# Kernel tuning notes

Measured on AMD Instinct MI355X. Metric: run time of the kernel, lower is better.

Reference implementation:

```python
import jax, jax.numpy as jnp
import numpy as np

HIDDEN_DIM = 64
EIGS_DIM = 16
N_LAYERS = 2
NUM_USERS = 100000
NUM_ITEMS = 200000
N_NODES = NUM_USERS + NUM_ITEMS
N_EDGES = 1250000
N_PATHS = 14  # 2**(sample_hop+1) - 2 with sample_hop=3
LN_EPS = 1e-5


def setup_inputs() -> dict:
    key = jax.random.key(0)
    k1, k2, k3, k4, k5 = jax.random.split(key, 5)
    return {
        "user_emb": 0.1 * jax.random.normal(k1, (NUM_USERS, HIDDEN_DIM), dtype=jnp.float32),
        "item_emb": 0.1 * jax.random.normal(k2, (NUM_ITEMS, HIDDEN_DIM), dtype=jnp.float32),
        "eigs": jax.random.normal(k3, (N_NODES, EIGS_DIM), dtype=jnp.float32),
        "lambda0": jnp.zeros((N_LAYERS,), dtype=jnp.float32),
        "path_emb_w": jnp.zeros((N_LAYERS, N_PATHS, 1), dtype=jnp.float32),
        "indices": jax.random.randint(k4, (2, N_EDGES), 0, N_NODES, dtype=jnp.int64)
        if jax.config.jax_enable_x64
        else jax.random.randint(k4, (2, N_EDGES), 0, N_NODES, dtype=jnp.int32),
        "path_type": jax.random.randint(k5, (N_EDGES,), 0, N_PATHS, dtype=jnp.int32),
    }


def _layer_norm(x, eps=LN_EPS):
    mu = jnp.mean(x, axis=-1, keepdims=True)
    var = jnp.var(x, axis=-1, keepdims=True)
    return (x - mu) * jax.lax.rsqrt(var + eps)


def _sparse_softmax(row, s, num_nodes):
    # softmax over edges grouped by target-node row index
    m = jax.ops.segment_max(s, row, num_segments=num_nodes)
    e = jnp.exp(s - m[row])
    denom = jax.ops.segment_sum(e, row, num_segments=num_nodes)
    return e / denom[row]


def _attention(y, eigs, row, col, path_type, lam0, pemb):
    sqrt_dim = 1.0 / jnp.sqrt(jnp.float32(HIDDEN_DIM))
    # per-edge q.k score  [E]
    x = jnp.sum(y[row] * y[col], axis=-1) * sqrt_dim
    yeig = jnp.sum(eigs[row] * eigs[col], axis=-1)
    s0 = x + jnp.exp(lam0) * yeig
    s1 = pemb[path_type, 0]
    a0 = _sparse_softmax(row, s0, N_NODES)
    a1 = _sparse_softmax(row, s1, N_NODES)
    a = 0.5 * (a0 + a1)
    # sparse-dense matmul: out[r] = sum_e a_e * v[col_e]
    return jax.ops.segment_sum(a[:, None] * y[col], row, num_segments=N_NODES)


def reference(user_emb, item_emb, eigs, lambda0, path_emb_w, indices, path_type):
    row, col = indices[0], indices[1]
    all_emb = jnp.concatenate([user_emb, item_emb], axis=0)  # [N, d]
    embs = [all_emb]
    for l in range(N_LAYERS):
        y = _layer_norm(all_emb)
        all_emb = _attention(y, eigs, row, col, path_type, lambda0[l], path_emb_w[l])
        embs.append(all_emb)
    light_out = jnp.mean(jnp.stack(embs, axis=1), axis=1)  # [N, d]
    return light_out
```

## Files before the change

### kernel.cpp

```cpp
#include <hip/hip_runtime.h>
#include <hip/hip_bf16.h>

#define HD 64
#define ED 16
#define NU 100000
#define NI 200000
#define NN 300000
#define NE 1250000
#define NP 14

#define RB 512
#define NBKT ((NN + RB - 1) / RB)
#define NR8 (NBKT * RB)
#define A_ITEMS 16
#define A_CHUNK (256 * A_ITEMS)
#define A_BLOCKS ((NE + A_CHUNK - 1) / A_CHUNK)
#define DBINS 64

typedef __hip_bfloat16 bf16;
typedef unsigned short ushort8v __attribute__((ext_vector_type(8)));

__device__ __forceinline__ float bf2f(unsigned short u) {
    union { unsigned int i; float f; } c; c.i = ((unsigned int)u) << 16; return c.f;
}
__device__ __forceinline__ unsigned short f2b(float x) {
    bf16 h = __float2bfloat16(x);
    unsigned short u; __builtin_memcpy(&u, &h, 2); return u;
}

__global__ void ln_kernel(const float* __restrict__ user_emb,
                          const float* __restrict__ item_emb,
                          const float* __restrict__ eigs,
                          bf16* __restrict__ yb,
                          bf16* __restrict__ eb)
{
    const int tid = blockIdx.x * blockDim.x + threadIdx.x;
    const int r   = tid >> 3;
    const int sub = tid & 7;
    if (r >= NN) return;
    const float* src = (r < NU) ? user_emb + (size_t)r * HD
                                : item_emb + (size_t)(r - NU) * HD;
    const float4 lo = *reinterpret_cast<const float4*>(src + sub * 8);
    const float4 hi = *reinterpret_cast<const float4*>(src + sub * 8 + 4);
    float x[8] = {lo.x, lo.y, lo.z, lo.w, hi.x, hi.y, hi.z, hi.w};

    float sm = 0.0f, sq = 0.0f;
#pragma unroll
    for (int j = 0; j < 8; ++j) { sm += x[j]; sq += x[j] * x[j]; }
    sm += __shfl_xor(sm, 1, 64); sq += __shfl_xor(sq, 1, 64);
    sm += __shfl_xor(sm, 2, 64); sq += __shfl_xor(sq, 2, 64);
    sm += __shfl_xor(sm, 4, 64); sq += __shfl_xor(sq, 4, 64);
    const float mu  = sm * (1.0f / 64.0f);
    const float var = sq * (1.0f / 64.0f) - mu * mu;
    const float inv = rsqrtf(var + 1e-5f);

    ushort8v w;
#pragma unroll
    for (int j = 0; j < 8; ++j) w[j] = f2b((x[j] - mu) * inv);
    *reinterpret_cast<ushort8v*>(yb + (size_t)r * HD + sub * 8) = w;

    const float2 ev = *reinterpret_cast<const float2*>(eigs + (size_t)r * ED + sub * 2);
    const unsigned int packed = (unsigned int)f2b(ev.x) | ((unsigned int)f2b(ev.y) << 16);
    *reinterpret_cast<unsigned int*>(eb + (size_t)r * ED + sub * 2) = packed;
}

__global__ void bkt_count_kernel(const int* __restrict__ row,
                                 int* __restrict__ bkt_cnt)
{
    __shared__ int hist[NBKT];
    const int tid = threadIdx.x;
    for (int j = tid; j < NBKT; j += 256) hist[j] = 0;
    __syncthreads();
    const int base = blockIdx.x * A_CHUNK;
#pragma unroll
    for (int i = 0; i < A_ITEMS; ++i) {
        const int idx = base + i * 256 + tid;
        if (idx < NE) atomicAdd(&hist[row[idx] >> 9], 1);
    }
    __syncthreads();
    for (int j = tid; j < NBKT; j += 256) {
        const int h = hist[j];
        if (h) atomicAdd(&bkt_cnt[j], h);
    }
}

__global__ void bkt_scan_kernel(const int* __restrict__ bkt_cnt,
                                int* __restrict__ bkt_base,
                                int* __restrict__ wq_bkt)
{
    __shared__ int s[1024];
    const int t = threadIdx.x;
    const int v = (t < NBKT) ? bkt_cnt[t] : 0;
    s[t] = v;
    __syncthreads();
    for (int off = 1; off < 1024; off <<= 1) {
        int x = (t >= off) ? s[t - off] : 0;
        __syncthreads();
        s[t] += x;
        __syncthreads();
    }
    if (t < NBKT) {
        const int excl = s[t] - v;
        bkt_base[t] = excl;
        wq_bkt[t]   = excl;
        if (t == NBKT - 1) bkt_base[NBKT] = s[t];
    }
}

__global__ void bkt_scatter_kernel(const int* __restrict__ row,
                                   const int* __restrict__ col,
                                   const int* __restrict__ pt,
                                   int* __restrict__ wq_bkt,
                                   int* __restrict__ pairs)
{
    __shared__ int hist[NBKT];
    __shared__ int rbase[NBKT];
    __shared__ int roff[NBKT];
    const int tid = threadIdx.x;
    for (int j = tid; j < NBKT; j += 256) { hist[j] = 0; roff[j] = 0; }
    __syncthreads();

    const int base = blockIdx.x * A_CHUNK;
#pragma unroll
    for (int i = 0; i < A_ITEMS; ++i) {
        const int idx = base + i * 256 + tid;
        if (idx < NE) atomicAdd(&hist[row[idx] >> 9], 1);
    }
    __syncthreads();
    for (int j = tid; j < NBKT; j += 256) {
        const int h = hist[j];
        if (h) rbase[j] = atomicAdd(&wq_bkt[j], h);
    }
    __syncthreads();
#pragma unroll
    for (int i = 0; i < A_ITEMS; ++i) {
        const int idx = base + i * 256 + tid;
        if (idx < NE) {
            const int r = row[idx];
            const int b = r >> 9;
            const int v = col[idx] | (pt[idx] << 19) | ((r & (RB - 1)) << 23);
            const int o = atomicAdd(&roff[b], 1);
            pairs[rbase[b] + o] = v;
        }
    }
}

__global__ void bkt_sort_kernel(const int* __restrict__ bkt_base,
                                const int* __restrict__ pairs,
                                const float* __restrict__ eigs,
                                const bf16* __restrict__ eb,
                                int2* __restrict__ rinfo,
                                int2* __restrict__ epacked)
{
    __shared__ int rcnt[RB], lrp[RB], wq2[RB], ssum[256];
    __shared__ int dhist[DBINS], dbase[DBINS];
    __shared__ int perml[RB];
    __shared__ float estage[RB * ED];
    const int tid = threadIdx.x;
    const int b   = blockIdx.x;
    const int r0  = b * RB;
    const int s   = bkt_base[b];
    const int e   = bkt_base[b + 1];

    for (int j = tid; j < RB; j += 256) { rcnt[j] = 0; wq2[j] = 0; perml[j] = -1; }
    for (int j = tid; j < DBINS; j += 256) dhist[j] = 0;
    for (int k = tid; k < RB * ED; k += 256) {
        const int g = r0 * ED + k;
        estage[k] = (g < NN * ED) ? eigs[g] : 0.0f;
    }
    __syncthreads();

    for (int i = s + tid; i < e; i += 256)
        atomicAdd(&rcnt[(pairs[i] >> 23) & (RB - 1)], 1);
    __syncthreads();

    const int a0 = rcnt[2 * tid], a1 = rcnt[2 * tid + 1];
    ssum[tid] = a0 + a1;
    __syncthreads();
    for (int off = 1; off < 256; off <<= 1) {
        int x = (tid >= off) ? ssum[tid - off] : 0;
        __syncthreads();
        ssum[tid] += x;
        __syncthreads();
    }
    const int excl = ssum[tid] - (a0 + a1);
    lrp[2 * tid]     = excl;
    lrp[2 * tid + 1] = excl + a0;
    __syncthreads();

    const int ra   = r0 + 2 * tid;
    const int bin0 = (a0 < DBINS - 1) ? a0 : (DBINS - 1);
    const int bin1 = (a1 < DBINS - 1) ? a1 : (DBINS - 1);
    if (ra < NN)     atomicAdd(&dhist[bin0], 1);
    if (ra + 1 < NN) atomicAdd(&dhist[bin1], 1);
    __syncthreads();
    ssum[tid] = (tid < DBINS) ? dhist[tid] : 0;
    __syncthreads();
    for (int off = 1; off < DBINS; off <<= 1) {
        int x = (tid >= off) ? ssum[tid - off] : 0;
        __syncthreads();
        ssum[tid] += x;
        __syncthreads();
    }
    if (tid < DBINS) { dbase[tid] = ssum[tid] - dhist[tid]; dhist[tid] = 0; }
    __syncthreads();
    if (ra < NN)     perml[dbase[bin0] + atomicAdd(&dhist[bin0], 1)] = 2 * tid;
    if (ra + 1 < NN) perml[dbase[bin1] + atomicAdd(&dhist[bin1], 1)] = 2 * tid + 1;
    __syncthreads();

    for (int j = tid; j < RB; j += 256) {
        const int rl = perml[j];
        int2 out;
        if (rl >= 0) {
            int dg = rcnt[rl]; if (dg > 0xFFF) dg = 0xFFF;
            out = make_int2(s + lrp[rl], (r0 + rl) | (dg << 19));
        } else {
            out = make_int2(0, -1);
        }
        rinfo[r0 + j] = out;
    }

    for (int i = s + tid; i < e; i += 256) {
        const int v  = pairs[i];
        const int rl = (v >> 23) & (RB - 1);
        const int c  = v & 0x7FFFF;
        const ushort8v* ep = reinterpret_cast<const ushort8v*>(eb + (size_t)c * ED);
        const ushort8v q0 = ep[0], q1 = ep[1];
        const float* er = estage + rl * ED;
        float d = 0.0f;
#pragma unroll
        for (int j = 0; j < 8; ++j) d += bf2f(q0[j]) * er[j];
#pragma unroll
        for (int j = 0; j < 8; ++j) d += bf2f(q1[j]) * er[j + 8];
        const int o   = atomicAdd(&wq2[rl], 1);
        const int pos = s + lrp[rl] + o;
        epacked[pos] = make_int2(v & 0x7FFFFF, __float_as_int(d));
    }
}

template <int LAYER>
__global__ __launch_bounds__(256, 4)
void attn_row_kernel(const bf16* __restrict__ yb,
                     const int2* __restrict__ rinfo,
                     const int2* __restrict__ epacked,
                     const float* __restrict__ lambda0,
                     const float* __restrict__ pemb,
                     const float* __restrict__ user_emb,
                     const float* __restrict__ item_emb,
                     bf16* __restrict__ yb_next,
                     float* __restrict__ io)
{
    __shared__ float e1tab[NP];
    if (threadIdx.x < NP)
        e1tab[threadIdx.x] = __expf(pemb[LAYER * NP + threadIdx.x]);
    __syncthreads();

    const int tid  = blockIdx.x * blockDim.x + threadIdx.x;
    const int g    = tid >> 3;
    const int sub  = tid & 7;
    const int lane = (int)(threadIdx.x & 63);
    const int2 ri  = rinfo[g];
    if (ri.y < 0) return;
    const int r    = ri.y & 0x7FFFF;
    const int deg  = (ri.y >> 19) & 0xFFF;
    if (LAYER == 1 && deg == 0) return;

    const int start = ri.x;
    const float lam = __expf(lambda0[LAYER]);

    float yrf[8];
    {
        ushort8v u = *reinterpret_cast<const ushort8v*>(yb + (size_t)r * HD + sub * 8);
#pragma unroll
        for (int j = 0; j < 8; ++j) yrf[j] = bf2f(u[j]);
    }

    float U0[8], U1[8];
#pragma unroll
    for (int j = 0; j < 8; ++j) { U0[j] = 0.0f; U1[j] = 0.0f; }
    float d0 = 0.0f, d1 = 0.0f;

    const bf16* ybs = yb + (size_t)sub * 8;

    int2 myv = (sub < deg) ? epacked[start + sub] : make_int2(0, 0);
    for (int k0 = 0; k0 < deg; k0 += 8) {
        const bool more = (k0 + 8) < deg;
        int2 nxt = make_int2(0, 0);
        if (more && (k0 + 8 + sub) < deg) nxt = epacked[start + k0 + 8 + sub];

        int   vv[8];
        float ee[8];
#pragma unroll
        for (int kk = 0; kk < 8; ++kk) {
            const int src = (lane & ~7) + kk;
            vv[kk] = __shfl(myv.x, src, 64);
            ee[kk] = __int_as_float(__shfl(myv.y, src, 64));
        }

        const int nb = ((deg - k0) < 8) ? (deg - k0) : 8;

        const bf16* p0 = ybs + (size_t)(vv[0] & 0x7FFFF) * HD;
        const bf16* p1 = ybs + (size_t)(vv[1] & 0x7FFFF) * HD;
        const bf16* p2 = ybs + (size_t)(vv[2] & 0x7FFFF) * HD;
        const bf16* p3 = ybs + (size_t)(vv[3] & 0x7FFFF) * HD;
        const bf16* p4 = ybs + (size_t)(vv[4] & 0x7FFFF) * HD;
        const bf16* p5 = ybs + (size_t)(vv[5] & 0x7FFFF) * HD;
        const bf16* p6 = ybs + (size_t)(vv[6] & 0x7FFFF) * HD;
        const bf16* p7 = ybs + (size_t)(vv[7] & 0x7FFFF) * HD;
        ushort8v u0, u1, u2, u3, u4, u5, u6, u7;
        asm volatile("global_load_dwordx4 %0, %1, off" : "=v"(u0) : "v"(p0));
        asm volatile("global_load_dwordx4 %0, %1, off" : "=v"(u1) : "v"(p1));
        asm volatile("global_load_dwordx4 %0, %1, off" : "=v"(u2) : "v"(p2));
        asm volatile("global_load_dwordx4 %0, %1, off" : "=v"(u3) : "v"(p3));
        asm volatile("global_load_dwordx4 %0, %1, off" : "=v"(u4) : "v"(p4));
        asm volatile("global_load_dwordx4 %0, %1, off" : "=v"(u5) : "v"(p5));
        asm volatile("global_load_dwordx4 %0, %1, off" : "=v"(u6) : "v"(p6));
        asm volatile("global_load_dwordx4 %0, %1, off" : "=v"(u7) : "v"(p7));
        asm volatile("s_waitcnt vmcnt(0)"
                     : "+v"(u0), "+v"(u1), "+v"(u2), "+v"(u3),
                       "+v"(u4), "+v"(u5), "+v"(u6), "+v"(u7));

        auto consume = [&](const ushort8v& uc, int vk, float ek) {
            float yc[8];
            float sdot = 0.0f;
#pragma unroll
            for (int j = 0; j < 8; ++j) { yc[j] = bf2f(uc[j]); sdot += yrf[j] * yc[j]; }
            sdot += __shfl_xor(sdot, 1, 64);
            sdot += __shfl_xor(sdot, 2, 64);
            sdot += __shfl_xor(sdot, 4, 64);
            const float e0 = __expf(sdot * 0.125f + lam * ek);
            const float e1 = e1tab[(vk >> 19) & 15];
            d0 += e0; d1 += e1;
#pragma unroll
            for (int j = 0; j < 8; ++j) {
                U0[j] += e0 * yc[j];
                U1[j] += e1 * yc[j];
            }
        };
        if (nb > 0) consume(u0, vv[0], ee[0]);
        if (nb > 1) consume(u1, vv[1], ee[1]);
        if (nb > 2) consume(u2, vv[2], ee[2]);
        if (nb > 3) consume(u3, vv[3], ee[3]);
        if (nb > 4) consume(u4, vv[4], ee[4]);
        if (nb > 5) consume(u5, vv[5], ee[5]);
        if (nb > 6) consume(u6, vv[6], ee[6]);
        if (nb > 7) consume(u7, vv[7], ee[7]);

        myv = nxt;
    }

    const float i0 = deg ? 0.5f / d0 : 0.0f;
    const float i1 = deg ? 0.5f / d1 : 0.0f;
    float acc[8];
#pragma unroll
    for (int j = 0; j < 8; ++j) acc[j] = i0 * U0[j] + i1 * U1[j];

    float* iorow = io + (size_t)r * HD + sub * 8;
    if (LAYER == 0) {
        float sm = 0.0f, sq = 0.0f;
#pragma unroll
        for (int j = 0; j < 8; ++j) { sm += acc[j]; sq += acc[j] * acc[j]; }
        sm += __shfl_xor(sm, 1, 64); sq += __shfl_xor(sq, 1, 64);
        sm += __shfl_xor(sm, 2, 64); sq += __shfl_xor(sq, 2, 64);
        sm += __shfl_xor(sm, 4, 64); sq += __shfl_xor(sq, 4, 64);
        const float mu  = sm * (1.0f / 64.0f);
        const float var = sq * (1.0f / 64.0f) - mu * mu;
        const float inv = rsqrtf(var + 1e-5f);
        ushort8v w;
#pragma unroll
        for (int j = 0; j < 8; ++j) w[j] = f2b((acc[j] - mu) * inv);
        *reinterpret_cast<ushort8v*>(yb_next + (size_t)r * HD + sub * 8) = w;

        const float* e0p = (r < NU) ? user_emb + (size_t)r * HD + sub * 8
                                    : item_emb + (size_t)(r - NU) * HD + sub * 8;
        const float4 lo = *reinterpret_cast<const float4*>(e0p);
        const float4 hi = *reinterpret_cast<const float4*>(e0p + 4);
        const float third = 1.0f / 3.0f;
        *reinterpret_cast<float4*>(iorow) =
            make_float4((lo.x + acc[0]) * third, (lo.y + acc[1]) * third,
                        (lo.z + acc[2]) * third, (lo.w + acc[3]) * third);
        *reinterpret_cast<float4*>(iorow + 4) =
            make_float4((hi.x + acc[4]) * third, (hi.y + acc[5]) * third,
                        (hi.z + acc[6]) * third, (hi.w + acc[7]) * third);
    } else {
        const float third = 1.0f / 3.0f;
        float4 lo = *reinterpret_cast<const float4*>(iorow);
        float4 hi = *reinterpret_cast<const float4*>(iorow + 4);
        lo.x += acc[0] * third; lo.y += acc[1] * third;
        lo.z += acc[2] * third; lo.w += acc[3] * third;
        hi.x += acc[4] * third; hi.y += acc[5] * third;
        hi.z += acc[6] * third; hi.w += acc[7] * third;
        *reinterpret_cast<float4*>(iorow)     = lo;
        *reinterpret_cast<float4*>(iorow + 4) = hi;
    }
}

extern "C" void kernel_launch(void* const* d_in, const int* in_sizes, int n_in,
                              void* d_out, int out_size, void* d_ws, size_t ws_size,
                              hipStream_t stream)
{
    const float* user_emb = (const float*)d_in[0];
    const float* item_emb = (const float*)d_in[1];
    const float* eigs     = (const float*)d_in[2];
    const float* lambda0  = (const float*)d_in[3];
    const float* pemb     = (const float*)d_in[4];
    const int*   indices  = (const int*)d_in[5];
    const int*   ptype    = (const int*)d_in[6];
    const int*   row = indices;
    const int*   col = indices + NE;

    float* io = (float*)d_out;
    char*  ws = (char*)d_ws;
    bf16* yb       = (bf16*)ws;
    bf16* yb2      = yb + (size_t)NN * HD;
    bf16* eb       = yb2 + (size_t)NN * HD;
    int*  pairs    = (int*)(eb + (size_t)NN * ED);
    int2* epacked  = (int2*)(pairs + NE);
    int2* rinfo    = epacked + NE;
    int*  bkt_cnt  = (int*)(rinfo + NR8);
    int*  bkt_base = bkt_cnt + NBKT;
    int*  wq_bkt   = bkt_base + NBKT + 1;

    const dim3 blk(256);
    const int grid8 = (NR8 * 8) / 256;

    ln_kernel<<<(NN * 8 + 255) / 256, blk, 0, stream>>>(user_emb, item_emb, eigs, yb, eb);

    hipMemsetAsync(bkt_cnt, 0, NBKT * sizeof(int), stream);
    bkt_count_kernel<<<A_BLOCKS, blk, 0, stream>>>(row, bkt_cnt);
    bkt_scan_kernel<<<1, 1024, 0, stream>>>(bkt_cnt, bkt_base, wq_bkt);
    bkt_scatter_kernel<<<A_BLOCKS, blk, 0, stream>>>(row, col, ptype, wq_bkt, pairs);
    bkt_sort_kernel<<<NBKT, blk, 0, stream>>>(bkt_base, pairs, eigs, eb,
                                              rinfo, epacked);

    attn_row_kernel<0><<<grid8, blk, 0, stream>>>(yb, rinfo, epacked,
                                                  lambda0, pemb, user_emb,
                                                  item_emb, yb2, io);
    attn_row_kernel<1><<<grid8, blk, 0, stream>>>(yb2, rinfo, epacked,
                                                  lambda0, pemb, user_emb,
                                                  item_emb, nullptr, io);
}
```

Baseline: 405.9 us.

## Process four rows per 8-lane group with prefetched edges and descending-degree ordering

```diff
diff --git a/kernel.cpp b/kernel.cpp
--- a/kernel.cpp
+++ b/kernel.cpp
@@ -16,9 +16,12 @@
 #define A_CHUNK (256 * A_ITEMS)
 #define A_BLOCKS ((NE + A_CHUNK - 1) / A_CHUNK)
 #define DBINS 64
+#define IT 4
 
 typedef __hip_bfloat16 bf16;
 typedef unsigned short ushort8v __attribute__((ext_vector_type(8)));
+typedef float  float4v __attribute__((ext_vector_type(4)));
+typedef int    int2v   __attribute__((ext_vector_type(2)));
 
 __device__ __forceinline__ float bf2f(unsigned short u) {
     union { unsigned int i; float f; } c; c.i = ((unsigned int)u) << 16; return c.f;
@@ -189,8 +192,8 @@
     __syncthreads();
 
     const int ra   = r0 + 2 * tid;
-    const int bin0 = (a0 < DBINS - 1) ? a0 : (DBINS - 1);
-    const int bin1 = (a1 < DBINS - 1) ? a1 : (DBINS - 1);
+    const int bin0 = (DBINS - 1) - ((a0 < DBINS - 1) ? a0 : (DBINS - 1));
+    const int bin1 = (DBINS - 1) - ((a1 < DBINS - 1) ? a1 : (DBINS - 1));
     if (ra < NN)     atomicAdd(&dhist[bin0], 1);
     if (ra + 1 < NN) atomicAdd(&dhist[bin1], 1);
     __syncthreads();
@@ -255,49 +258,60 @@
         e1tab[threadIdx.x] = __expf(pemb[LAYER * NP + threadIdx.x]);
     __syncthreads();
 
-    const int tid  = blockIdx.x * blockDim.x + threadIdx.x;
-    const int g    = tid >> 3;
+    const int tid  = (int)threadIdx.x;
+    const int gl   = tid >> 3;
     const int sub  = tid & 7;
-    const int lane = (int)(threadIdx.x & 63);
-    const int2 ri  = rinfo[g];
-    if (ri.y < 0) return;
-    const int r    = ri.y & 0x7FFFF;
-    const int deg  = (ri.y >> 19) & 0xFFF;
-    if (LAYER == 1 && deg == 0) return;
-
-    const int start = ri.x;
+    const int lane = tid & 63;
+    const int base = (int)blockIdx.x * (32 * IT);
+
     const float lam = __expf(lambda0[LAYER]);
-
-    float yrf[8];
+    const bf16*  ybs = yb + (size_t)sub * 8;
+    const int2v* ep2 = reinterpret_cast<const int2v*>(epacked);
+
+    int2 ri[IT];
+#pragma unroll
+    for (int it = 0; it < IT; ++it) ri[it] = rinfo[base + it * 32 + gl];
+
+    int2v myv_n;
     {
-        ushort8v u = *reinterpret_cast<const ushort8v*>(yb + (size_t)r * HD + sub * 8);
-#pragma unroll
-        for (int j = 0; j < 8; ++j) yrf[j] = bf2f(u[j]);
-    }
-
-    float U0[8], U1[8];
-#pragma unroll
-    for (int j = 0; j < 8; ++j) { U0[j] = 0.0f; U1[j] = 0.0f; }
-    float d0 = 0.0f, d1 = 0.0f;
-
-    const bf16* ybs = yb + (size_t)sub * 8;
-
-    int2 myv = (sub < deg) ? epacked[start + sub] : make_int2(0, 0);
-    for (int k0 = 0; k0 < deg; k0 += 8) {
-        const bool more = (k0 + 8) < deg;
-        int2 nxt = make_int2(0, 0);
-        if (more && (k0 + 8 + sub) < deg) nxt = epacked[start + k0 + 8 + sub];
+        const int2v* mp = ep2 + ri[0].x + sub;
+        asm volatile("global_load_dwordx2 %0, %1, off" : "=v"(myv_n) : "v"(mp));
+        asm volatile("s_waitcnt vmcnt(0)" : "+v"(myv_n));
+    }
+
+#pragma unroll
+    for (int it = 0; it < IT; ++it) {
+        const int2 ric   = ri[it];
+        const bool valid = (ric.y >= 0);
+        const int r      = valid ? (ric.y & 0x7FFFF) : 0;
+        const int deg    = valid ? ((ric.y >> 19) & 0xFFF) : 0;
+        const int start  = ric.x;
+
+        int2v myv = myv_n;
+        if (sub >= deg) { myv[0] = 0; myv[1] = 0; }
 
         int   vv[8];
         float ee[8];
 #pragma unroll
         for (int kk = 0; kk < 8; ++kk) {
             const int src = (lane & ~7) + kk;
-            vv[kk] = __shfl(myv.x, src, 64);
-            ee[kk] = __int_as_float(__shfl(myv.y, src, 64));
-        }
-
-        const int nb = ((deg - k0) < 8) ? (deg - k0) : 8;
+            vv[kk] = __shfl(myv[0], src, 64);
+            ee[kk] = __int_as_float(__shfl(myv[1], src, 64));
+        }
+        const int nb = (deg < 8) ? deg : 8;
+
+        ushort8v yru;
+        float4v em_lo, em_hi;
+        {
+            const bf16* yp = ybs + (size_t)r * HD;
+            asm volatile("global_load_dwordx4 %0, %1, off" : "=v"(yru) : "v"(yp));
+            const float* ep = (LAYER == 0)
+                ? (((r < NU) ? user_emb + (size_t)r * HD
+                             : item_emb + (size_t)(r - NU) * HD) + sub * 8)
+                : (io + (size_t)r * HD + sub * 8);
+            asm volatile("global_load_dwordx4 %0, %1, off" : "=v"(em_lo) : "v"(ep));
+            asm volatile("global_load_dwordx4 %0, %1, off" : "=v"(em_hi) : "v"(ep + 4));
+        }
 
         const bf16* p0 = ybs + (size_t)(vv[0] & 0x7FFFF) * HD;
         const bf16* p1 = ybs + (size_t)(vv[1] & 0x7FFFF) * HD;
@@ -316,9 +330,25 @@
         asm volatile("global_load_dwordx4 %0, %1, off" : "=v"(u5) : "v"(p5));
         asm volatile("global_load_dwordx4 %0, %1, off" : "=v"(u6) : "v"(p6));
         asm volatile("global_load_dwordx4 %0, %1, off" : "=v"(u7) : "v"(p7));
+
+        if (it + 1 < IT) {
+            const int2v* mp = ep2 + ri[it + 1].x + sub;
+            asm volatile("global_load_dwordx2 %0, %1, off" : "=v"(myv_n) : "v"(mp));
+        }
+
         asm volatile("s_waitcnt vmcnt(0)"
                      : "+v"(u0), "+v"(u1), "+v"(u2), "+v"(u3),
-                       "+v"(u4), "+v"(u5), "+v"(u6), "+v"(u7));
+                       "+v"(u4), "+v"(u5), "+v"(u6), "+v"(u7),
+                       "+v"(yru), "+v"(em_lo), "+v"(em_hi), "+v"(myv_n));
+
+        float yrf[8];
+#pragma unroll
+        for (int j = 0; j < 8; ++j) yrf[j] = bf2f(yru[j]);
+
+        float U0[8], U1[8];
+#pragma unroll
+        for (int j = 0; j < 8; ++j) { U0[j] = 0.0f; U1[j] = 0.0f; }
+        float d0 = 0.0f, d1 = 0.0f;
 
         auto consume = [&](const ushort8v& uc, int vk, float ek) {
             float yc[8];
@@ -346,52 +376,72 @@
         if (nb > 6) consume(u6, vv[6], ee[6]);
         if (nb > 7) consume(u7, vv[7], ee[7]);
 
-        myv = nxt;
-    }
-
-    const float i0 = deg ? 0.5f / d0 : 0.0f;
-    const float i1 = deg ? 0.5f / d1 : 0.0f;
-    float acc[8];
-#pragma unroll
-    for (int j = 0; j < 8; ++j) acc[j] = i0 * U0[j] + i1 * U1[j];
-
-    float* iorow = io + (size_t)r * HD + sub * 8;
-    if (LAYER == 0) {
-        float sm = 0.0f, sq = 0.0f;
-#pragma unroll
-        for (int j = 0; j < 8; ++j) { sm += acc[j]; sq += acc[j] * acc[j]; }
-        sm += __shfl_xor(sm, 1, 64); sq += __shfl_xor(sq, 1, 64);
-        sm += __shfl_xor(sm, 2, 64); sq += __shfl_xor(sq, 2, 64);
-        sm += __shfl_xor(sm, 4, 64); sq += __shfl_xor(sq, 4, 64);
-        const float mu  = sm * (1.0f / 64.0f);
-        const float var = sq * (1.0f / 64.0f) - mu * mu;
-        const float inv = rsqrtf(var + 1e-5f);
-        ushort8v w;
-#pragma unroll
-        for (int j = 0; j < 8; ++j) w[j] = f2b((acc[j] - mu) * inv);
-        *reinterpret_cast<ushort8v*>(yb_next + (size_t)r * HD + sub * 8) = w;
-
-        const float* e0p = (r < NU) ? user_emb + (size_t)r * HD + sub * 8
-                                    : item_emb + (size_t)(r - NU) * HD + sub * 8;
-        const float4 lo = *reinterpret_cast<const float4*>(e0p);
-        const float4 hi = *reinterpret_cast<const float4*>(e0p + 4);
-        const float third = 1.0f / 3.0f;
-        *reinterpret_cast<float4*>(iorow) =
-            make_float4((lo.x + acc[0]) * third, (lo.y + acc[1]) * third,
-                        (lo.z + acc[2]) * third, (lo.w + acc[3]) * third);
-        *reinterpret_cast<float4*>(iorow + 4) =
-            make_float4((hi.x + acc[4]) * third, (hi.y + acc[5]) * third,
-                        (hi.z + acc[6]) * third, (hi.w + acc[7]) * third);
-    } else {
-        const float third = 1.0f / 3.0f;
-        float4 lo = *reinterpret_cast<const float4*>(iorow);
-        float4 hi = *reinterpret_cast<const float4*>(iorow + 4);
-        lo.x += acc[0] * third; lo.y += acc[1] * third;
-        lo.z += acc[2] * third; lo.w += acc[3] * third;
-        hi.x += acc[4] * third; hi.y += acc[5] * third;
-        hi.z += acc[6] * third; hi.w += acc[7] * third;
-        *reinterpret_cast<float4*>(iorow)     = lo;
-        *reinterpret_cast<float4*>(iorow + 4) = hi;
+        for (int k0 = 8; k0 < deg; k0 += 8) {
+            int2 mv = ((k0 + sub) < deg) ? epacked[start + k0 + sub]
+                                         : make_int2(0, 0);
+            int   vv2[8];
+            float ee2[8];
+#pragma unroll
+            for (int kk = 0; kk < 8; ++kk) {
+                const int src = (lane & ~7) + kk;
+                vv2[kk] = __shfl(mv.x, src, 64);
+                ee2[kk] = __int_as_float(__shfl(mv.y, src, 64));
+            }
+            const int nb2 = ((deg - k0) < 8) ? (deg - k0) : 8;
+#pragma unroll
+            for (int kk = 0; kk < 8; ++kk) {
+                if (kk < nb2) {
+                    ushort8v uc = *reinterpret_cast<const ushort8v*>(
+                        ybs + (size_t)(vv2[kk] & 0x7FFFF) * HD);
+                    consume(uc, vv2[kk], ee2[kk]);
+                }
+            }
+        }
+
+        const float i0 = deg ? 0.5f / d0 : 0.0f;
+        const float i1 = deg ? 0.5f / d1 : 0.0f;
+        float acc[8];
+#pragma unroll
+        for (int j = 0; j < 8; ++j) acc[j] = i0 * U0[j] + i1 * U1[j];
+
+        float* iorow = io + (size_t)r * HD + sub * 8;
+        if (LAYER == 0) {
+            if (valid) {
+                float sm = 0.0f, sq = 0.0f;
+#pragma unroll
+                for (int j = 0; j < 8; ++j) { sm += acc[j]; sq += acc[j] * acc[j]; }
+                sm += __shfl_xor(sm, 1, 64); sq += __shfl_xor(sq, 1, 64);
+                sm += __shfl_xor(sm, 2, 64); sq += __shfl_xor(sq, 2, 64);
+                sm += __shfl_xor(sm, 4, 64); sq += __shfl_xor(sq, 4, 64);
+                const float mu  = sm * (1.0f / 64.0f);
+                const float var = sq * (1.0f / 64.0f) - mu * mu;
+                const float inv = rsqrtf(var + 1e-5f);
+                ushort8v w;
+#pragma unroll
+                for (int j = 0; j < 8; ++j) w[j] = f2b((acc[j] - mu) * inv);
+                *reinterpret_cast<ushort8v*>(yb_next + (size_t)r * HD + sub * 8) = w;
+
+                const float third = 1.0f / 3.0f;
+                float4v o0, o1;
+                o0[0] = (em_lo[0] + acc[0]) * third; o0[1] = (em_lo[1] + acc[1]) * third;
+                o0[2] = (em_lo[2] + acc[2]) * third; o0[3] = (em_lo[3] + acc[3]) * third;
+                o1[0] = (em_hi[0] + acc[4]) * third; o1[1] = (em_hi[1] + acc[5]) * third;
+                o1[2] = (em_hi[2] + acc[6]) * third; o1[3] = (em_hi[3] + acc[7]) * third;
+                *reinterpret_cast<float4v*>(iorow)     = o0;
+                *reinterpret_cast<float4v*>(iorow + 4) = o1;
+            }
+        } else {
+            if (valid && deg > 0) {
+                const float third = 1.0f / 3.0f;
+                float4v o0, o1;
+                o0[0] = em_lo[0] + acc[0] * third; o0[1] = em_lo[1] + acc[1] * third;
+                o0[2] = em_lo[2] + acc[2] * third; o0[3] = em_lo[3] + acc[3] * third;
+                o1[0] = em_hi[0] + acc[4] * third; o1[1] = em_hi[1] + acc[5] * third;
+                o1[2] = em_hi[2] + acc[6] * third; o1[3] = em_hi[3] + acc[7] * third;
+                *reinterpret_cast<float4v*>(iorow)     = o0;
+                *reinterpret_cast<float4v*>(iorow + 4) = o1;
+            }
+        }
     }
 }
 
@@ -422,7 +472,7 @@
     int*  wq_bkt   = bkt_base + NBKT + 1;
 
     const dim3 blk(256);
-    const int grid8 = (NR8 * 8) / 256;
+    const int gridAttn = NR8 / (32 * IT);
 
     ln_kernel<<<(NN * 8 + 255) / 256, blk, 0, stream>>>(user_emb, item_emb, eigs, yb, eb);
 
@@ -433,10 +483,10 @@
     bkt_sort_kernel<<<NBKT, blk, 0, stream>>>(bkt_base, pairs, eigs, eb,
                                               rinfo, epacked);
 
-    attn_row_kernel<0><<<grid8, blk, 0, stream>>>(yb, rinfo, epacked,
-                                                  lambda0, pemb, user_emb,
-                                                  item_emb, yb2, io);
-    attn_row_kernel<1><<<grid8, blk, 0, stream>>>(yb2, rinfo, epacked,
-                                                  lambda0, pemb, user_emb,
-                                                  item_emb, nullptr, io);
-}
+    attn_row_kernel<0><<<gridAttn, blk, 0, stream>>>(yb, rinfo, epacked,
+                                                     lambda0, pemb, user_emb,
+                                                     item_emb, yb2, io);
+    attn_row_kernel<1><<<gridAttn, blk, 0, stream>>>(yb2, rinfo, epacked,
+                                                     lambda0, pemb, user_emb,
+                                                     item_emb, nullptr, io);
+}
```

Measured after the change: 401.1 us. No clear change (-1.2%).
